# Optimization experiments

Hardware: AMD Instinct MI355X
Metric: run time of the kernel (lower is better)

Reference implementation:

```python
import jax, jax.numpy as jnp
import numpy as np

NUM_EXPERTS = 8
TOP_K = 2


def setup_inputs() -> dict:
    key = jax.random.key(0)
    ks = jax.random.split(key, 5)
    B, S, H, F, E = 4, 2048, 1024, 4096, NUM_EXPERTS
    scale_h = 1.0 / np.sqrt(H)
    scale_f = 1.0 / np.sqrt(F)
    return {
        "hidden_states": jax.random.normal(ks[0], (B, S, H), dtype=jnp.float32),
        "Wr": jax.random.normal(ks[1], (H, E), dtype=jnp.float32) * scale_h,
        "br": jnp.zeros((E,), dtype=jnp.float32),
        "W1": jax.random.normal(ks[2], (E, H, F), dtype=jnp.float32) * scale_h,
        "b1": jnp.zeros((E, F), dtype=jnp.float32),
        "W2": jax.random.normal(ks[3], (E, F, H), dtype=jnp.float32) * scale_f,
        "b2": jnp.zeros((E, H), dtype=jnp.float32),
    }


def _moe_forward(x, Wr, br, W1, b1, W2, b2):
    B, S, H = x.shape
    T = B * S
    xf = x.reshape(T, H)
    # Router: softmax over expert logits, take top-k, renormalize weights.
    logits = xf @ Wr + br                      # [T, E]
    probs = jax.nn.softmax(logits, axis=-1)
    top_p, top_i = jax.lax.top_k(probs, TOP_K)  # [T, K]
    weights = top_p / jnp.sum(top_p, axis=-1, keepdims=True)
    # combine[t, e] = sum_k weights[t,k] * (top_i[t,k] == e)
    one_hot = jax.nn.one_hot(top_i, NUM_EXPERTS, dtype=xf.dtype)  # [T, K, E]
    combine = jnp.einsum("tk,tke->te", weights, one_hot)          # [T, E]
    # Per-expert FFN (loop over small fixed expert count); weighted sum.
    out = jnp.zeros_like(xf)
    for e in range(NUM_EXPERTS):
        h = jax.nn.gelu(xf @ W1[e] + b1[e], approximate=False)    # [T, F]
        y = h @ W2[e] + b2[e]                                     # [T, H]
        out = out + combine[:, e:e + 1] * y
    return out.reshape(B, S, H)


def reference(hidden_states, Wr, br, W1, b1, W2, b2):
    return _moe_forward(hidden_states, Wr, br, W1, b1, W2, b2)
```

## Files before the change

### kernel.cpp

```cpp
#include <hip/hip_runtime.h>
#include <cstdint>
#include <cmath>

#define T_TOK 8192
#define H_DIM 1024
#define F_DIM 4096
#define NE 8
#define CAP 8192
#define BK 64
#define BM 128
#define BN 256
#define BN2 128
#define MBLK 32
#define LDK 140
#define RTOK 32

typedef __attribute__((ext_vector_type(8))) short short8v;
typedef __attribute__((ext_vector_type(4))) float f32x4;

static __device__ __forceinline__ unsigned short f2bf(float f) {
    union { float f; unsigned int u; } v; v.f = f;
    unsigned int r = v.u + 0x7FFFu + ((v.u >> 16) & 1u);
    return (unsigned short)(r >> 16);
}

static __device__ __forceinline__ float bf2f(unsigned short u) {
    union { unsigned int i; float f; } v; v.i = ((unsigned)u) << 16; return v.f;
}

static __device__ __forceinline__ float fast_gelu(float x) {
    const float s  = x * 0.70710678118f;
    const float as = fabsf(s);
    const float t  = __builtin_amdgcn_rcpf(fmaf(0.3275911f, as, 1.f));
    float p = fmaf(1.061405429f, t, -1.453152027f);
    p = fmaf(p, t, 1.421413741f);
    p = fmaf(p, t, -0.284496736f);
    p = fmaf(p, t, 0.254829592f);
    p = p * t;
    const float E = __expf(-as * as);
    const float erf_abs = fmaf(-p, E, 1.f);
    const float erf_s = copysignf(erf_abs, s);
    return 0.5f * x * (1.f + erf_s);
}

static __device__ __forceinline__ void gl_lds16(const void* g, void* l) {
    __builtin_amdgcn_global_load_lds(
        (const __attribute__((address_space(1))) unsigned int*)g,
        (__attribute__((address_space(3))) unsigned int*)l, 16, 0, 0);
}

static __device__ __forceinline__ int prefix128(const int* cnt, int e) {
    int o = 0;
    for (int q = 0; q < e; ++q) o += ((cnt[q] + 127) >> 7) << 7;
    return o;
}

static __device__ __forceinline__ void transpose_tile(
    const float* __restrict__ in, unsigned short* __restrict__ out,
    int R, int C, int e, int bx, int by, unsigned short* tile_s)
{
    const int r0 = by * 128, c0 = bx * 64;
    const int colg = threadIdx.x & 15;
    const int rowg = threadIdx.x >> 4;
    const float* ip = in + (size_t)e * R * C + (size_t)r0 * C + c0;
#pragma unroll
    for (int p = 0; p < 2; ++p) {
        const int rr = (rowg + p * 16) * 4;
        const float4 v0 = *(const float4*)(ip + (size_t)(rr + 0) * C + colg * 4);
        const float4 v1 = *(const float4*)(ip + (size_t)(rr + 1) * C + colg * 4);
        const float4 v2 = *(const float4*)(ip + (size_t)(rr + 2) * C + colg * 4);
        const float4 v3 = *(const float4*)(ip + (size_t)(rr + 3) * C + colg * 4);
        const float rv[4][4] = {{v0.x, v0.y, v0.z, v0.w}, {v1.x, v1.y, v1.z, v1.w},
                                {v2.x, v2.y, v2.z, v2.w}, {v3.x, v3.y, v3.z, v3.w}};
#pragma unroll
        for (int ci = 0; ci < 4; ++ci) {
            ushort4 o;
            o.x = f2bf(rv[0][ci]); o.y = f2bf(rv[1][ci]);
            o.z = f2bf(rv[2][ci]); o.w = f2bf(rv[3][ci]);
            *(ushort4*)(tile_s + (colg * 4 + ci) * LDK + rr) = o;
        }
    }
    __syncthreads();
    unsigned short* op = out + (size_t)e * R * C + (size_t)c0 * R + r0;
#pragma unroll
    for (int p = 0; p < 4; ++p) {
        const int c = (threadIdx.x >> 4) + p * 16;
        const int s = (threadIdx.x & 15) * 8;
        const unsigned short* sp = tile_s + c * LDK + s;
        const uint2 w0 = *(const uint2*)(sp);
        const uint2 w1 = *(const uint2*)(sp + 4);
        uint4 o4; o4.x = w0.x; o4.y = w0.y; o4.z = w1.x; o4.w = w1.y;
        *(uint4*)(op + (size_t)c * R + s) = o4;
    }
}

#define G_ROUT (T_TOK / RTOK)
#define G_TC   4096

__global__ __launch_bounds__(256) void prep_k(
    const float* __restrict__ x, const float* __restrict__ Wr,
    const float* __restrict__ br, const float* __restrict__ W1,
    int* __restrict__ cnt, int* __restrict__ perm,
    int* __restrict__ inv, float* __restrict__ tw,
    unsigned short* __restrict__ xb, unsigned short* __restrict__ w1t)
{
    __shared__ __align__(16) unsigned short tile_s[64 * LDK];
    __shared__ int   sh_e01[RTOK];
    __shared__ float sh_w0[RTOK];
    __shared__ int   sh_r0[RTOK], sh_r1[RTOK];
    __shared__ int   lcnt[NE], gbase[NE];
    const int bid = blockIdx.x;
    const int tid = threadIdx.x;

    if (bid >= G_ROUT) {
        const int j = bid - G_ROUT;
        const int e = j >> 9; const int rem = j & 511;
        transpose_tile(W1, w1t, H_DIM, F_DIM, e, rem >> 3, rem & 7, tile_s);
        return;
    }

    const int wave = tid >> 6;
    const int lane = tid & 63;
    if (tid < NE) lcnt[tid] = 0;
    __syncthreads();

    for (int tk = 0; tk < RTOK / 4; ++tk) {
        const int li = wave * (RTOK / 4) + tk;
        const int t = bid * RTOK + li;
        const float* xr = x + (size_t)t * H_DIM;
        float acc[NE];
#pragma unroll
        for (int e = 0; e < NE; ++e) acc[e] = 0.f;
#pragma unroll
        for (int c0 = 0; c0 < H_DIM; c0 += 256) {
            const float4 v = *(const float4*)(xr + c0 + lane * 4);
            ushort4 ob;
            ob.x = f2bf(v.x); ob.y = f2bf(v.y); ob.z = f2bf(v.z); ob.w = f2bf(v.w);
            *(ushort4*)(xb + (size_t)t * H_DIM + c0 + lane * 4) = ob;
            const int hbase = c0 + lane * 4;
            float vv[4] = {v.x, v.y, v.z, v.w};
#pragma unroll
            for (int i = 0; i < 4; ++i) {
                const float4 w0 = *(const float4*)(Wr + (size_t)(hbase + i) * NE);
                const float4 w1 = *(const float4*)(Wr + (size_t)(hbase + i) * NE + 4);
                acc[0] += vv[i] * w0.x; acc[1] += vv[i] * w0.y;
                acc[2] += vv[i] * w0.z; acc[3] += vv[i] * w0.w;
                acc[4] += vv[i] * w1.x; acc[5] += vv[i] * w1.y;
                acc[6] += vv[i] * w1.z; acc[7] += vv[i] * w1.w;
            }
        }
#pragma unroll
        for (int off = 32; off > 0; off >>= 1) {
#pragma unroll
            for (int e = 0; e < NE; ++e) acc[e] += __shfl_xor(acc[e], off, 64);
        }
        if (lane == 0) {
#pragma unroll
            for (int e = 0; e < NE; ++e) acc[e] += br[e];
            int i0 = 0; float l0 = acc[0];
#pragma unroll
            for (int e = 1; e < NE; ++e) if (acc[e] > l0) { l0 = acc[e]; i0 = e; }
            int i1 = -1; float l1 = -3.4e38f;
#pragma unroll
            for (int e = 0; e < NE; ++e) if (e != i0 && acc[e] > l1) { l1 = acc[e]; i1 = e; }
            sh_e01[li] = (i0 << 3) | i1;
            sh_w0[li] = 1.f / (1.f + expf(l1 - l0));
        }
    }
    __syncthreads();

    if (tid < RTOK) {
        const int e0 = sh_e01[tid] >> 3, e1 = sh_e01[tid] & 7;
        sh_r0[tid] = atomicAdd(&lcnt[e0], 1);
        sh_r1[tid] = atomicAdd(&lcnt[e1], 1);
    }
    __syncthreads();
    if (tid < NE) gbase[tid] = atomicAdd(&cnt[tid], lcnt[tid]);
    __syncthreads();
    if (tid < RTOK) {
        const int t = bid * RTOK + tid;
        const int e0 = sh_e01[tid] >> 3, e1 = sh_e01[tid] & 7;
        const int p0 = gbase[e0] + sh_r0[tid];
        const int p1 = gbase[e1] + sh_r1[tid];
        const float w0 = sh_w0[tid];
        perm[e0 * CAP + p0] = t;
        perm[e1 * CAP + p1] = t;
        inv[2 * t + 0] = (e0 << 13) | p0;  tw[2 * t + 0] = w0;
        inv[2 * t + 1] = (e1 << 13) | p1;  tw[2 * t + 1] = 1.f - w0;
    }
}

__global__ __launch_bounds__(256, 2) void gemm1_k(
    const unsigned short* __restrict__ xb,
    const unsigned short* __restrict__ w1t,
    const float* __restrict__ b1,
    const float* __restrict__ W2,
    unsigned short* __restrict__ w2t,
    unsigned short* __restrict__ hbuf,
    const int* __restrict__ perm, const int* __restrict__ cnt)
{
    __shared__ __align__(16) unsigned short smem[(BM + BN) * BK];
    __shared__ int rows_s[BM];

    const int bid = blockIdx.x;

    {
        const int e2 = bid >> 9; const int rem2 = bid & 511;
        transpose_tile(W2, w2t, F_DIM, H_DIM, e2, rem2 >> 5, rem2 & 31, smem);
    }

    constexpr int NY = F_DIM / BN;
    constexpr int nwg = MBLK * NY * NE;
    const int wg = (bid & 7) * (nwg >> 3) + (bid >> 3);
    const int e  = wg / (MBLK * NY);
    const int rem = wg % (MBLK * NY);
    const int nb = rem / MBLK;
    const int mb = rem % MBLK;

    const int c = cnt[e];
    const int m0 = mb * BM;
    const int tid = threadIdx.x;
    if (m0 >= c) return;

    if (tid < BM) {
        const int i = m0 + tid;
        rows_s[tid] = perm[e * CAP + (i < c ? i : c - 1)];
    }
    __syncthreads();

    const int lane = tid & 63;
    const int w = tid >> 6;
    const int srow = tid >> 3;
    const int u = tid & 7;
    const int us = (u ^ (srow & 7)) * 8;

    const unsigned short* bp = w1t + ((size_t)e * F_DIM + nb * BN) * H_DIM;
    const unsigned short* srcA[4];
    const unsigned short* srcB[8];
    int dstA[4], dstB[8];
#pragma unroll
    for (int j = 0; j < 4; ++j) {
        srcA[j] = xb + (size_t)rows_s[j * 32 + srow] * H_DIM + us;
        dstA[j] = (j * 32 + w * 8) * BK + lane * 8;
    }
#pragma unroll
    for (int j = 0; j < 8; ++j) {
        srcB[j] = bp + (size_t)(j * 32 + srow) * H_DIM + us;
        dstB[j] = BM * BK + (j * 32 + w * 8) * BK + lane * 8;
    }

    f32x4 acc[4][8];
#pragma unroll
    for (int m = 0; m < 4; ++m)
#pragma unroll
        for (int n = 0; n < 8; ++n) acc[m][n] = (f32x4){0.f, 0.f, 0.f, 0.f};

    const int wm = w >> 1;
    const int wn = w & 1;
    const int fr = lane & 15;
    const int fg = lane >> 4;
    const int fx = fr & 7;

    for (int k0 = 0; k0 < H_DIM; k0 += BK) {
#pragma unroll
        for (int j = 0; j < 4; ++j) gl_lds16(srcA[j] + k0, smem + dstA[j]);
#pragma unroll
        for (int j = 0; j < 8; ++j) gl_lds16(srcB[j] + k0, smem + dstB[j]);
        __syncthreads();
        const unsigned short* A = smem;
        const unsigned short* B = smem + BM * BK;
#pragma unroll
        for (int kk = 0; kk < 2; ++kk) {
            const int q = kk * 4 + fg;
            const int ua = (q ^ fx) * 8;
            short8v a[4], b[8];
#pragma unroll
            for (int m = 0; m < 4; ++m)
                a[m] = *(const short8v*)(A + (wm * 64 + m * 16 + fr) * BK + ua);
#pragma unroll
            for (int n = 0; n < 8; ++n)
                b[n] = *(const short8v*)(B + (wn * 128 + n * 16 + fr) * BK + ua);
#pragma unroll
            for (int m = 0; m < 4; ++m)
#pragma unroll
                for (int n = 0; n < 8; ++n)
                    acc[m][n] = __builtin_amdgcn_mfma_f32_16x16x32_bf16(b[n], a[m], acc[m][n], 0, 0, 0);
        }
        __syncthreads();
    }

    const size_t hrow0 = (size_t)prefix128(cnt, e) + m0;
#pragma unroll
    for (int n = 0; n < 8; ++n) {
        const int f = nb * BN + wn * 128 + n * 16 + fg * 4;
        const float4 bv = *(const float4*)(b1 + e * F_DIM + f);
        const float bb[4] = {bv.x, bv.y, bv.z, bv.w};
#pragma unroll
        for (int m = 0; m < 4; ++m) {
            const int tl = wm * 64 + m * 16 + fr;
            ushort4 o;
#pragma unroll
            for (int r = 0; r < 4; ++r) {
                const float g = fast_gelu(acc[m][n][r] + bb[r]);
                ((unsigned short*)&o)[r] = f2bf(g);
            }
            *(ushort4*)(hbuf + (hrow0 + tl) * F_DIM + f) = o;
        }
    }
}

__global__ __launch_bounds__(256, 2) void gemm2_k(
    const unsigned short* __restrict__ hbuf,
    const unsigned short* __restrict__ w2t,
    const float* __restrict__ b2,
    unsigned short* __restrict__ ybuf,
    const int* __restrict__ cnt)
{
    __shared__ __align__(16) unsigned short smem[(BM + BN2) * BK];

    constexpr int NY = H_DIM / BN2;
    constexpr int nwg = MBLK * NY * NE;
    const int bid = blockIdx.x;
    const int wg = (bid & 7) * (nwg >> 3) + (bid >> 3);
    const int e  = wg / (MBLK * NY);
    const int rem = wg % (MBLK * NY);
    const int nb = rem / MBLK;
    const int mb = rem % MBLK;

    const int c = cnt[e];
    const int m0 = mb * BM;
    if (m0 >= c) return;
    const int tid = threadIdx.x;

    const int lane = tid & 63;
    const int w = tid >> 6;
    const int srow = tid >> 3;
    const int u = tid & 7;
    const int us = (u ^ (srow & 7)) * 8;

    const size_t arow0 = (size_t)prefix128(cnt, e) + m0;
    const unsigned short* bp = w2t + ((size_t)e * H_DIM + nb * BN2) * F_DIM;
    const unsigned short* srcA[4];
    const unsigned short* srcB[4];
    int dstA[4], dstB[4];
#pragma unroll
    for (int j = 0; j < 4; ++j) {
        srcA[j] = hbuf + (arow0 + j * 32 + srow) * F_DIM + us;
        dstA[j] = (j * 32 + w * 8) * BK + lane * 8;
        srcB[j] = bp + (size_t)(j * 32 + srow) * F_DIM + us;
        dstB[j] = BM * BK + dstA[j];
    }

    f32x4 acc[4][4];
#pragma unroll
    for (int m = 0; m < 4; ++m)
#pragma unroll
        for (int n = 0; n < 4; ++n) acc[m][n] = (f32x4){0.f, 0.f, 0.f, 0.f};

    const int wr = (tid >> 7) & 1;
    const int wc = (tid >> 6) & 1;
    const int fr = lane & 15;
    const int fg = lane >> 4;
    const int fx = fr & 7;

    for (int k0 = 0; k0 < F_DIM; k0 += BK) {
#pragma unroll
        for (int j = 0; j < 4; ++j) gl_lds16(srcA[j] + k0, smem + dstA[j]);
#pragma unroll
        for (int j = 0; j < 4; ++j) gl_lds16(srcB[j] + k0, smem + dstB[j]);
        __syncthreads();
        const unsigned short* A = smem;
        const unsigned short* B = smem + BM * BK;
#pragma unroll
        for (int kk = 0; kk < 2; ++kk) {
            const int q = kk * 4 + fg;
            const int ua = (q ^ fx) * 8;
            short8v a[4], b[4];
#pragma unroll
            for (int m = 0; m < 4; ++m)
                a[m] = *(const short8v*)(A + (wr * 64 + m * 16 + fr) * BK + ua);
#pragma unroll
            for (int n = 0; n < 4; ++n)
                b[n] = *(const short8v*)(B + (wc * 64 + n * 16 + fr) * BK + ua);
#pragma unroll
            for (int m = 0; m < 4; ++m)
#pragma unroll
                for (int n = 0; n < 4; ++n)
                    acc[m][n] = __builtin_amdgcn_mfma_f32_16x16x32_bf16(b[n], a[m], acc[m][n], 0, 0, 0);
        }
        __syncthreads();
    }

#pragma unroll
    for (int n = 0; n < 4; ++n) {
        const int h = nb * BN2 + wc * 64 + n * 16 + fg * 4;
        const float4 bv = *(const float4*)(b2 + e * H_DIM + h);
#pragma unroll
        for (int m = 0; m < 4; ++m) {
            const int tl = wr * 64 + m * 16 + fr;
            ushort4 o;
            o.x = f2bf(acc[m][n][0] + bv.x);
            o.y = f2bf(acc[m][n][1] + bv.y);
            o.z = f2bf(acc[m][n][2] + bv.z);
            o.w = f2bf(acc[m][n][3] + bv.w);
            *(ushort4*)(ybuf + (arow0 + tl) * H_DIM + h) = o;
        }
    }
}

__global__ __launch_bounds__(256) void combine_k(
    const unsigned short* __restrict__ ybuf, const int* __restrict__ inv,
    const float* __restrict__ tw, const int* __restrict__ cnt,
    float* __restrict__ out)
{
    const int t = blockIdx.x;
    const int j = threadIdx.x;
    const int i0 = inv[2 * t], i1 = inv[2 * t + 1];
    const float w0 = tw[2 * t], w1 = tw[2 * t + 1];
    const size_t r0 = (size_t)prefix128(cnt, i0 >> 13) + (i0 & 8191);
    const size_t r1 = (size_t)prefix128(cnt, i1 >> 13) + (i1 & 8191);
    const ushort4 a = *(const ushort4*)(ybuf + r0 * H_DIM + j * 4);
    const ushort4 b = *(const ushort4*)(ybuf + r1 * H_DIM + j * 4);
    float4 o;
    o.x = w0 * bf2f(a.x) + w1 * bf2f(b.x);
    o.y = w0 * bf2f(a.y) + w1 * bf2f(b.y);
    o.z = w0 * bf2f(a.z) + w1 * bf2f(b.z);
    o.w = w0 * bf2f(a.w) + w1 * bf2f(b.w);
    *(float4*)(out + (size_t)t * H_DIM + j * 4) = o;
}

extern "C" void kernel_launch(void* const* d_in, const int* in_sizes, int n_in,
                              void* d_out, int out_size, void* d_ws, size_t ws_size,
                              hipStream_t stream)
{
    const float* x  = (const float*)d_in[0];
    const float* Wr = (const float*)d_in[1];
    const float* br = (const float*)d_in[2];
    const float* W1 = (const float*)d_in[3];
    const float* b1 = (const float*)d_in[4];
    const float* W2 = (const float*)d_in[5];
    const float* b2 = (const float*)d_in[6];
    float* out = (float*)d_out;

    char* ws = (char*)d_ws;
    size_t off = 0;
    auto alloc = [&](size_t bytes) {
        char* p = ws + off;
        off += (bytes + 255) & ~(size_t)255;
        return p;
    };
    unsigned short* w2t  = (unsigned short*)alloc((size_t)NE * H_DIM * F_DIM * 2);
    unsigned short* w1t  = (unsigned short*)alloc((size_t)NE * F_DIM * H_DIM * 2);
    unsigned short* xb   = (unsigned short*)alloc((size_t)T_TOK * H_DIM * 2);
    unsigned short* hbuf = (unsigned short*)alloc((size_t)(T_TOK * 2 + NE * BM) * F_DIM * 2);
    int*   cnt  = (int*)alloc(NE * 4);
    int*   perm = (int*)alloc((size_t)NE * CAP * 4);
    int*   inv  = (int*)alloc((size_t)T_TOK * 2 * 4);
    float* tw   = (float*)alloc((size_t)T_TOK * 2 * 4);
    unsigned short* ybuf = w1t;
    (void)ws_size; (void)in_sizes; (void)n_in; (void)out_size;

    hipMemsetAsync(cnt, 0, NE * 4, stream);
    prep_k<<<G_ROUT + G_TC, 256, 0, stream>>>(x, Wr, br, W1, cnt, perm, inv, tw, xb, w1t);
    gemm1_k<<<MBLK * (F_DIM / BN) * NE, 256, 0, stream>>>(
        xb, w1t, b1, W2, w2t, hbuf, perm, cnt);
    gemm2_k<<<MBLK * (H_DIM / BN2) * NE, 256, 0, stream>>>(hbuf, w2t, b2, ybuf, cnt);
    combine_k<<<T_TOK, 256, 0, stream>>>(ybuf, inv, tw, cnt, out);
}
```

Before: 473.4 us.

## Double-buffer LDS tiles with async prefetch in both expert GEMMs

Both expert GEMM kernels move from a single-buffered BK=64 loop with full syncthreads to a double-buffered BK=32 pipeline. The next-but-one K tile is issued as direct global-to-LDS loads while MFMAs run on registers already read from the current buffer, using explicit vmcnt/lgkmcnt waits, raw barriers and setprio around the MFMA block. The goal is to hide global load latency behind the matrix math. In exchange there are twice as many K iterations and barriers per tile, and the swizzle is narrowed to a 4-way XOR, which may bring back some LDS bank conflicts.

```diff
diff --git a/kernel.cpp b/kernel.cpp
--- a/kernel.cpp
+++ b/kernel.cpp
@@ -7,16 +7,29 @@
 #define F_DIM 4096
 #define NE 8
 #define CAP 8192
-#define BK 64
+#define BK 32
 #define BM 128
 #define BN 256
 #define BN2 128
 #define MBLK 32
 #define LDK 140
 #define RTOK 32
+#define BUFSZ1 ((BM + BN) * BK)
+#define BUFSZ2 ((BM + BN2) * BK)
 
 typedef __attribute__((ext_vector_type(8))) short short8v;
 typedef __attribute__((ext_vector_type(4))) float f32x4;
+
+#define WAITV6 do { asm volatile("s_waitcnt vmcnt(6)" ::: "memory"); \
+                    __builtin_amdgcn_sched_barrier(0); } while (0)
+#define WAITV4 do { asm volatile("s_waitcnt vmcnt(4)" ::: "memory"); \
+                    __builtin_amdgcn_sched_barrier(0); } while (0)
+#define WAITV0 do { asm volatile("s_waitcnt vmcnt(0)" ::: "memory"); \
+                    __builtin_amdgcn_sched_barrier(0); } while (0)
+#define LGKM0  do { asm volatile("s_waitcnt lgkmcnt(0)" ::: "memory"); \
+                    __builtin_amdgcn_sched_barrier(0); } while (0)
+#define BAR    do { __builtin_amdgcn_s_barrier(); \
+                    __builtin_amdgcn_sched_barrier(0); } while (0)
 
 static __device__ __forceinline__ unsigned short f2bf(float f) {
     union { float f; unsigned int u; } v; v.f = f;
@@ -199,7 +212,7 @@
     unsigned short* __restrict__ hbuf,
     const int* __restrict__ perm, const int* __restrict__ cnt)
 {
-    __shared__ __align__(16) unsigned short smem[(BM + BN) * BK];
+    __shared__ __align__(16) unsigned short smem[2 * BUFSZ1];
     __shared__ int rows_s[BM];
 
     const int bid = blockIdx.x;
@@ -230,24 +243,25 @@
 
     const int lane = tid & 63;
     const int w = tid >> 6;
-    const int srow = tid >> 3;
-    const int u = tid & 7;
-    const int us = (u ^ (srow & 7)) * 8;
+    const int rq = lane >> 2;
+    const int usq = ((tid & 3) ^ (rq & 3)) * 8;
 
     const unsigned short* bp = w1t + ((size_t)e * F_DIM + nb * BN) * H_DIM;
-    const unsigned short* srcA[4];
-    const unsigned short* srcB[8];
-    int dstA[4], dstB[8];
-#pragma unroll
-    for (int j = 0; j < 4; ++j) {
-        srcA[j] = xb + (size_t)rows_s[j * 32 + srow] * H_DIM + us;
-        dstA[j] = (j * 32 + w * 8) * BK + lane * 8;
-    }
-#pragma unroll
-    for (int j = 0; j < 8; ++j) {
-        srcB[j] = bp + (size_t)(j * 32 + srow) * H_DIM + us;
-        dstB[j] = BM * BK + (j * 32 + w * 8) * BK + lane * 8;
-    }
+    const unsigned short* src[6];
+    int dst[6];
+#pragma unroll
+    for (int j = 0; j < 6; ++j) {
+        const int sr = j * 64 + 16 * w + rq;
+        src[j] = (j < 2) ? (xb + (size_t)rows_s[sr] * H_DIM + usq)
+                         : (bp + (size_t)(sr - BM) * H_DIM + usq);
+        dst[j] = (j * 64 + 16 * w) * BK + lane * 8;
+    }
+
+#define G1_STAGE(tt, bufoff) do {                                               \
+    const int _k = (tt) * BK;                                                   \
+    _Pragma("unroll") for (int j = 0; j < 6; ++j)                               \
+        gl_lds16(src[j] + _k, smem + (bufoff) + dst[j]);                        \
+} while (0)
 
     f32x4 acc[4][8];
 #pragma unroll
@@ -259,34 +273,46 @@
     const int wn = w & 1;
     const int fr = lane & 15;
     const int fg = lane >> 4;
-    const int fx = fr & 7;
-
-    for (int k0 = 0; k0 < H_DIM; k0 += BK) {
-#pragma unroll
-        for (int j = 0; j < 4; ++j) gl_lds16(srcA[j] + k0, smem + dstA[j]);
-#pragma unroll
-        for (int j = 0; j < 8; ++j) gl_lds16(srcB[j] + k0, smem + dstB[j]);
-        __syncthreads();
-        const unsigned short* A = smem;
-        const unsigned short* B = smem + BM * BK;
-#pragma unroll
-        for (int kk = 0; kk < 2; ++kk) {
-            const int q = kk * 4 + fg;
-            const int ua = (q ^ fx) * 8;
-            short8v a[4], b[8];
-#pragma unroll
-            for (int m = 0; m < 4; ++m)
-                a[m] = *(const short8v*)(A + (wm * 64 + m * 16 + fr) * BK + ua);
-#pragma unroll
-            for (int n = 0; n < 8; ++n)
-                b[n] = *(const short8v*)(B + (wn * 128 + n * 16 + fr) * BK + ua);
-#pragma unroll
-            for (int m = 0; m < 4; ++m)
-#pragma unroll
-                for (int n = 0; n < 8; ++n)
-                    acc[m][n] = __builtin_amdgcn_mfma_f32_16x16x32_bf16(b[n], a[m], acc[m][n], 0, 0, 0);
-        }
-        __syncthreads();
+    const int fs = (fg ^ (fr & 3)) * 8;
+
+#define G1_READ(curoff) do {                                                    \
+    _Pragma("unroll") for (int m = 0; m < 4; ++m)                               \
+        a[m] = *(const short8v*)(smem + (curoff) +                              \
+                                 (wm * 64 + m * 16 + fr) * BK + fs);            \
+    _Pragma("unroll") for (int n = 0; n < 8; ++n)                               \
+        b[n] = *(const short8v*)(smem + (curoff) +                              \
+                                 (BM + wn * 128 + n * 16 + fr) * BK + fs);      \
+} while (0)
+
+#define G1_MFMA do {                                                            \
+    __builtin_amdgcn_s_setprio(1);                                              \
+    _Pragma("unroll") for (int m = 0; m < 4; ++m)                               \
+        _Pragma("unroll") for (int n = 0; n < 8; ++n)                           \
+            acc[m][n] = __builtin_amdgcn_mfma_f32_16x16x32_bf16(                \
+                b[n], a[m], acc[m][n], 0, 0, 0);                                \
+    __builtin_amdgcn_s_setprio(0);                                              \
+} while (0)
+
+    constexpr int NT = H_DIM / BK;
+    G1_STAGE(0, 0); G1_STAGE(1, BUFSZ1);
+    for (int t = 0; t < NT - 1; ++t) {
+        WAITV6;
+        BAR;
+        const int cur = (t & 1) ? BUFSZ1 : 0;
+        short8v a[4], b[8];
+        G1_READ(cur);
+        LGKM0;
+        BAR;
+        if (t + 2 < NT) G1_STAGE(t + 2, cur);
+        G1_MFMA;
+    }
+    WAITV0; BAR;
+    {
+        const int cur = ((NT - 1) & 1) ? BUFSZ1 : 0;
+        short8v a[4], b[8];
+        G1_READ(cur);
+        LGKM0;
+        G1_MFMA;
     }
 
     const size_t hrow0 = (size_t)prefix128(cnt, e) + m0;
@@ -316,7 +342,7 @@
     unsigned short* __restrict__ ybuf,
     const int* __restrict__ cnt)
 {
-    __shared__ __align__(16) unsigned short smem[(BM + BN2) * BK];
+    __shared__ __align__(16) unsigned short smem[2 * BUFSZ2];
 
     constexpr int NY = H_DIM / BN2;
     constexpr int nwg = MBLK * NY * NE;
@@ -334,22 +360,26 @@
 
     const int lane = tid & 63;
     const int w = tid >> 6;
-    const int srow = tid >> 3;
-    const int u = tid & 7;
-    const int us = (u ^ (srow & 7)) * 8;
+    const int rq = lane >> 2;
+    const int usq = ((tid & 3) ^ (rq & 3)) * 8;
 
     const size_t arow0 = (size_t)prefix128(cnt, e) + m0;
     const unsigned short* bp = w2t + ((size_t)e * H_DIM + nb * BN2) * F_DIM;
-    const unsigned short* srcA[4];
-    const unsigned short* srcB[4];
-    int dstA[4], dstB[4];
+    const unsigned short* src[4];
+    int dst[4];
 #pragma unroll
     for (int j = 0; j < 4; ++j) {
-        srcA[j] = hbuf + (arow0 + j * 32 + srow) * F_DIM + us;
-        dstA[j] = (j * 32 + w * 8) * BK + lane * 8;
-        srcB[j] = bp + (size_t)(j * 32 + srow) * F_DIM + us;
-        dstB[j] = BM * BK + dstA[j];
-    }
+        const int sr = j * 64 + 16 * w + rq;
+        src[j] = (j < 2) ? (hbuf + (arow0 + sr) * F_DIM + usq)
+                         : (bp + (size_t)(sr - BM) * F_DIM + usq);
+        dst[j] = (j * 64 + 16 * w) * BK + lane * 8;
+    }
+
+#define G2_STAGE(tt, bufoff) do {                                               \
+    const int _k = (tt) * BK;                                                   \
+    _Pragma("unroll") for (int j = 0; j < 4; ++j)                               \
+        gl_lds16(src[j] + _k, smem + (bufoff) + dst[j]);                        \
+} while (0)
 
     f32x4 acc[4][4];
 #pragma unroll
@@ -361,34 +391,46 @@
     const int wc = (tid >> 6) & 1;
     const int fr = lane & 15;
     const int fg = lane >> 4;
-    const int fx = fr & 7;
-
-    for (int k0 = 0; k0 < F_DIM; k0 += BK) {
-#pragma unroll
-        for (int j = 0; j < 4; ++j) gl_lds16(srcA[j] + k0, smem + dstA[j]);
-#pragma unroll
-        for (int j = 0; j < 4; ++j) gl_lds16(srcB[j] + k0, smem + dstB[j]);
-        __syncthreads();
-        const unsigned short* A = smem;
-        const unsigned short* B = smem + BM * BK;
-#pragma unroll
-        for (int kk = 0; kk < 2; ++kk) {
-            const int q = kk * 4 + fg;
-            const int ua = (q ^ fx) * 8;
-            short8v a[4], b[4];
-#pragma unroll
-            for (int m = 0; m < 4; ++m)
-                a[m] = *(const short8v*)(A + (wr * 64 + m * 16 + fr) * BK + ua);
-#pragma unroll
-            for (int n = 0; n < 4; ++n)
-                b[n] = *(const short8v*)(B + (wc * 64 + n * 16 + fr) * BK + ua);
-#pragma unroll
-            for (int m = 0; m < 4; ++m)
-#pragma unroll
-                for (int n = 0; n < 4; ++n)
-                    acc[m][n] = __builtin_amdgcn_mfma_f32_16x16x32_bf16(b[n], a[m], acc[m][n], 0, 0, 0);
-        }
-        __syncthreads();
+    const int fs = (fg ^ (fr & 3)) * 8;
+
+#define G2_READ(curoff) do {                                                    \
+    _Pragma("unroll") for (int m = 0; m < 4; ++m)                               \
+        a[m] = *(const short8v*)(smem + (curoff) +                              \
+                                 (wr * 64 + m * 16 + fr) * BK + fs);            \
+    _Pragma("unroll") for (int n = 0; n < 4; ++n)                               \
+        b[n] = *(const short8v*)(smem + (curoff) +                              \
+                                 (BM + wc * 64 + n * 16 + fr) * BK + fs);       \
+} while (0)
+
+#define G2_MFMA do {                                                            \
+    __builtin_amdgcn_s_setprio(1);                                              \
+    _Pragma("unroll") for (int m = 0; m < 4; ++m)                               \
+        _Pragma("unroll") for (int n = 0; n < 4; ++n)                           \
+            acc[m][n] = __builtin_amdgcn_mfma_f32_16x16x32_bf16(                \
+                b[n], a[m], acc[m][n], 0, 0, 0);                                \
+    __builtin_amdgcn_s_setprio(0);                                              \
+} while (0)
+
+    constexpr int NT = F_DIM / BK;
+    G2_STAGE(0, 0); G2_STAGE(1, BUFSZ2);
+    for (int t = 0; t < NT - 1; ++t) {
+        WAITV4;
+        BAR;
+        const int cur = (t & 1) ? BUFSZ2 : 0;
+        short8v a[4], b[4];
+        G2_READ(cur);
+        LGKM0;
+        BAR;
+        if (t + 2 < NT) G2_STAGE(t + 2, cur);
+        G2_MFMA;
+    }
+    WAITV0; BAR;
+    {
+        const int cur = ((NT - 1) & 1) ? BUFSZ2 : 0;
+        short8v a[4], b[4];
+        G2_READ(cur);
+        LGKM0;
+        G2_MFMA;
     }
 
 #pragma unroll
```

Result: slower. 506.3 us (+7.0%).

## Distribute W2 transpose tiles through an atomic work queue in gemm1

Applied to the files above, without the earlier changes.

Before, every gemm1 block transposed one fixed W2 tile up front, ahead of its own GEMM work. Now idle blocks (those with no rows for their expert) and blocks that have finished their GEMM pull transpose tiles from a global atomic counter until all are done. The aim is to fill idle CUs and keep the transpose off the critical path of the GEMM. The cost is an atomic per tile, extra barriers, and a second memset launch.

```diff
diff --git a/kernel.cpp b/kernel.cpp
--- a/kernel.cpp
+++ b/kernel.cpp
@@ -197,17 +197,15 @@
     const float* __restrict__ W2,
     unsigned short* __restrict__ w2t,
     unsigned short* __restrict__ hbuf,
-    const int* __restrict__ perm, const int* __restrict__ cnt)
+    const int* __restrict__ perm, const int* __restrict__ cnt,
+    int* __restrict__ w2q)
 {
     __shared__ __align__(16) unsigned short smem[(BM + BN) * BK];
     __shared__ int rows_s[BM];
+    __shared__ int qs_s;
 
     const int bid = blockIdx.x;
-
-    {
-        const int e2 = bid >> 9; const int rem2 = bid & 511;
-        transpose_tile(W2, w2t, F_DIM, H_DIM, e2, rem2 >> 5, rem2 & 31, smem);
-    }
+    const int tid = threadIdx.x;
 
     constexpr int NY = F_DIM / BN;
     constexpr int nwg = MBLK * NY * NE;
@@ -219,8 +217,18 @@
 
     const int c = cnt[e];
     const int m0 = mb * BM;
-    const int tid = threadIdx.x;
-    if (m0 >= c) return;
+
+    if (m0 >= c) {
+        for (;;) {
+            if (tid == 0) qs_s = atomicAdd(w2q, 1);
+            __syncthreads();
+            const int s = qs_s;
+            if (s >= G_TC) return;
+            transpose_tile(W2, w2t, F_DIM, H_DIM, s >> 9, (s & 511) >> 5,
+                           (s & 511) & 31, smem);
+            __syncthreads();
+        }
+    }
 
     if (tid < BM) {
         const int i = m0 + tid;
@@ -306,6 +314,16 @@
             }
             *(ushort4*)(hbuf + (hrow0 + tl) * F_DIM + f) = o;
         }
+    }
+
+    for (;;) {
+        __syncthreads();
+        if (tid == 0) qs_s = atomicAdd(w2q, 1);
+        __syncthreads();
+        const int s = qs_s;
+        if (s >= G_TC) return;
+        transpose_tile(W2, w2t, F_DIM, H_DIM, s >> 9, (s & 511) >> 5,
+                       (s & 511) & 31, smem);
     }
 }
 
@@ -457,13 +475,15 @@
     int*   perm = (int*)alloc((size_t)NE * CAP * 4);
     int*   inv  = (int*)alloc((size_t)T_TOK * 2 * 4);
     float* tw   = (float*)alloc((size_t)T_TOK * 2 * 4);
+    int*   w2q  = (int*)alloc(4);
     unsigned short* ybuf = w1t;
     (void)ws_size; (void)in_sizes; (void)n_in; (void)out_size;
 
     hipMemsetAsync(cnt, 0, NE * 4, stream);
+    hipMemsetAsync(w2q, 0, 4, stream);
     prep_k<<<G_ROUT + G_TC, 256, 0, stream>>>(x, Wr, br, W1, cnt, perm, inv, tw, xb, w1t);
     gemm1_k<<<MBLK * (F_DIM / BN) * NE, 256, 0, stream>>>(
-        xb, w1t, b1, W2, w2t, hbuf, perm, cnt);
+        xb, w1t, b1, W2, w2t, hbuf, perm, cnt, w2q);
     gemm2_k<<<MBLK * (H_DIM / BN2) * NE, 256, 0, stream>>>(hbuf, w2t, b2, ybuf, cnt);
     combine_k<<<T_TOK, 256, 0, stream>>>(ybuf, inv, tw, cnt, out);
 }
```

Result: slower. 492.5 us (+4.0%).
